# Kernel tuning notes

Hardware: AMD Instinct MI355X
Metric: run time of the kernel (lower is better)

## Reference

```python
import jax, jax.numpy as jnp
import numpy as np

N, E, F_IN, H, T, G, NCONV = 50000, 800000, 128, 64, 8, 64, 3
BN_EPS = 1e-5


def _bn_relu(h, gamma, beta):
    # BatchNorm1d in training mode: biased batch stats over the node dim
    m = h.mean(axis=0)
    v = h.var(axis=0)
    return jax.nn.relu(gamma * (h - m) * jax.lax.rsqrt(v + BN_EPS) + beta)


def _mlp(h, W1, b1, g1, be1, W2, b2, g2, be2):
    h = _bn_relu(h @ W1 + b1, g1, be1)
    return _bn_relu(h @ W2 + b2, g2, be2)


def setup_inputs() -> dict:
    key = jax.random.key(0)
    ks = jax.random.split(key, 12)
    x = jax.random.normal(ks[0], (N, F_IN), dtype=jnp.float32)
    edge_index = jax.random.randint(ks[1], (2, E), 0, N, dtype=jnp.int64)
    batch = jnp.sort(jax.random.randint(ks[2], (N,), 0, G, dtype=jnp.int64))
    s = 0.05
    inp = {
        "x": x, "edge_index": edge_index, "batch": batch,
        # first_h: Linear(F_IN,H)+BN+ReLU+Linear(H,H)+BN+ReLU
        "fh_W1": jax.random.normal(ks[3], (F_IN, H), jnp.float32) * s,
        "fh_b1": jnp.zeros((H,), jnp.float32),
        "fh_g1": jnp.ones((H,), jnp.float32),
        "fh_be1": jnp.zeros((H,), jnp.float32),
        "fh_W2": jax.random.normal(ks[4], (H, H), jnp.float32) * s,
        "fh_b2": jnp.zeros((H,), jnp.float32),
        "fh_g2": jnp.ones((H,), jnp.float32),
        "fh_be2": jnp.zeros((H,), jnp.float32),
        # stacked GINConv MLPs (all H->H)
        "cv_W1": jax.random.normal(ks[5], (NCONV, H, H), jnp.float32) * s,
        "cv_b1": jnp.zeros((NCONV, H), jnp.float32),
        "cv_g1": jnp.ones((NCONV, H), jnp.float32),
        "cv_be1": jnp.zeros((NCONV, H), jnp.float32),
        "cv_W2": jax.random.normal(ks[6], (NCONV, H, H), jnp.float32) * s,
        "cv_b2": jnp.zeros((NCONV, H), jnp.float32),
        "cv_g2": jnp.ones((NCONV, H), jnp.float32),
        "cv_be2": jnp.zeros((NCONV, H), jnp.float32),
        # per-layer readout linears (NCONV+1 of them)
        "lin_W": jax.random.normal(ks[7], (NCONV + 1, H, T), jnp.float32) * s,
        "lin_b": jnp.zeros((NCONV + 1, T), jnp.float32),
    }
    return inp


def reference(x, edge_index, batch, fh_W1, fh_b1, fh_g1, fh_be1, fh_W2, fh_b2,
              fh_g2, fh_be2, cv_W1, cv_b1, cv_g1, cv_be1, cv_W2, cv_b2, cv_g2,
              cv_be2, lin_W, lin_b):
    src, dst = edge_index[0], edge_index[1]
    eps = 0.0  # eps=0.0, train_eps=False
    # layer 0: first_h + pooled readout
    h = _mlp(x, fh_W1, fh_b1, fh_g1, fh_be1, fh_W2, fh_b2, fh_g2, fh_be2)
    out = jax.ops.segment_max(h @ lin_W[0] + lin_b[0], batch, num_segments=G)
    # GIN conv layers: neighbor sum-aggregation + MLP, with per-layer readout
    for l in range(NCONV):
        agg = jax.ops.segment_sum(h[src], dst, num_segments=N)  # [N,H]
        h = _mlp((1.0 + eps) * h + agg, cv_W1[l], cv_b1[l], cv_g1[l],
                 cv_be1[l], cv_W2[l], cv_b2[l], cv_g2[l], cv_be2[l])
        out = out + jax.ops.segment_max(h @ lin_W[l + 1] + lin_b[l + 1],
                                        batch, num_segments=G)
    return (out, h)
```

## Files before the change

### kernel.cpp

```cpp
#include <hip/hip_runtime.h>
#include <hip/hip_fp16.h>

#define NN 50000
#define EE 800000
#define FIN 128
#define HH 64
#define TT 8
#define GG 64
#define NCONVS 3
#define BN_EPS 1e-5f
#define RNODES 128
#define NBKT 196
#define SCAT_CHUNK 2048

__device__ __forceinline__ unsigned enc_f32(float x) {
  unsigned u = __float_as_uint(x);
  return (u & 0x80000000u) ? ~u : (u | 0x80000000u);
}
__device__ __forceinline__ float dec_f32(unsigned e) {
  unsigned u = (e & 0x80000000u) ? (e & 0x7fffffffu) : ~e;
  return __uint_as_float(u);
}

template <int K, int MODE>
__global__ __launch_bounds__(256) void mm_stats_kernel(
    const float* __restrict__ in, const __half* __restrict__ hin,
    const __half* __restrict__ agg, const float* __restrict__ stats_in,
    const float* __restrict__ gamma, const float* __restrict__ beta,
    const float* __restrict__ W, const float* __restrict__ bias,
    __half* __restrict__ y16, float* __restrict__ stats_out) {
  constexpr int NPH = K / 64;
  __shared__ float Wl[K * HH];
  __shared__ float AT[64 * 68];
  __shared__ float ssl[128];
  __shared__ float sred[4][128];
  const int t = threadIdx.x;
  if (MODE == 1) {
    if (t < 64) {
      const float inv = 1.f / (float)NN;
      const float mean = stats_in[t] * inv;
      const float var = stats_in[64 + t] * inv - mean * mean;
      const float sc = gamma[t] * rsqrtf(var + BN_EPS);
      ssl[t] = sc;
      ssl[64 + t] = fmaf(-mean, sc, beta[t]);
    }
    __syncthreads();
  }
  {
    const float4* W4 = (const float4*)W;
    float4* Wl4 = (float4*)Wl;
#pragma unroll
    for (int i = 0; i < (K * HH) / 1024; ++i) Wl4[t + i * 256] = W4[t + i * 256];
  }
  const int srow = t >> 2, scq = t & 3;
  const int grow_s = blockIdx.x * 64 + srow;
  const int g4 = (t & 15) * 4;
  const int r0 = (t >> 4) * 4;
  const int row0 = blockIdx.x * 64 + r0;
  const float4 bb = *(const float4*)&bias[g4];
  float4 acc0 = make_float4(0, 0, 0, 0), acc1 = make_float4(0, 0, 0, 0);
  float4 acc2 = make_float4(0, 0, 0, 0), acc3 = make_float4(0, 0, 0, 0);

#pragma unroll
  for (int p = 0; p < NPH; ++p) {
    if (p > 0) __syncthreads();
    if (MODE == 0) {
      if (grow_s < NN) {
#pragma unroll
        for (int i = 0; i < 4; ++i) {
          const int kl = scq * 16 + i * 4;
          const float4 v = *(const float4*)&in[(size_t)grow_s * K + p * 64 + kl];
          AT[(kl + 0) * 68 + srow] = v.x;
          AT[(kl + 1) * 68 + srow] = v.y;
          AT[(kl + 2) * 68 + srow] = v.z;
          AT[(kl + 3) * 68 + srow] = v.w;
        }
      } else {
#pragma unroll
        for (int i = 0; i < 16; ++i) AT[(scq * 16 + i) * 68 + srow] = 0.f;
      }
    } else {
      if (grow_s < NN) {
#pragma unroll
        for (int q = 0; q < 2; ++q) {
          const int kl = scq * 16 + q * 8;
          const int4 rv = *(const int4*)&hin[grow_s * HH + kl];
          const __half2* hp = (const __half2*)&rv;
          const float2 f0 = __half22float2(hp[0]);
          const float2 f1 = __half22float2(hp[1]);
          const float2 f2 = __half22float2(hp[2]);
          const float2 f3 = __half22float2(hp[3]);
          float f[8] = {f0.x, f0.y, f1.x, f1.y, f2.x, f2.y, f3.x, f3.y};
          if (MODE == 2) {
            const int4 av = *(const int4*)&agg[grow_s * HH + kl];
            const __half2* ap = (const __half2*)&av;
            const float2 a0 = __half22float2(ap[0]);
            const float2 a1 = __half22float2(ap[1]);
            const float2 a2 = __half22float2(ap[2]);
            const float2 a3 = __half22float2(ap[3]);
            f[0] += a0.x; f[1] += a0.y; f[2] += a1.x; f[3] += a1.y;
            f[4] += a2.x; f[5] += a2.y; f[6] += a3.x; f[7] += a3.y;
          } else {
#pragma unroll
            for (int j = 0; j < 8; ++j)
              f[j] = fmaxf(fmaf(f[j], ssl[kl + j], ssl[64 + kl + j]), 0.f);
          }
#pragma unroll
          for (int j = 0; j < 8; ++j) AT[(kl + j) * 68 + srow] = f[j];
        }
      } else {
#pragma unroll
        for (int i = 0; i < 16; ++i) AT[(scq * 16 + i) * 68 + srow] = 0.f;
      }
    }
    __syncthreads();
#pragma unroll 8
    for (int kl = 0; kl < 64; ++kl) {
      const float4 w = *(const float4*)&Wl[(p * 64 + kl) * HH + g4];
      const float4 a = *(const float4*)&AT[kl * 68 + r0];
      acc0.x = fmaf(a.x, w.x, acc0.x); acc0.y = fmaf(a.x, w.y, acc0.y);
      acc0.z = fmaf(a.x, w.z, acc0.z); acc0.w = fmaf(a.x, w.w, acc0.w);
      acc1.x = fmaf(a.y, w.x, acc1.x); acc1.y = fmaf(a.y, w.y, acc1.y);
      acc1.z = fmaf(a.y, w.z, acc1.z); acc1.w = fmaf(a.y, w.w, acc1.w);
      acc2.x = fmaf(a.z, w.x, acc2.x); acc2.y = fmaf(a.z, w.y, acc2.y);
      acc2.z = fmaf(a.z, w.z, acc2.z); acc2.w = fmaf(a.z, w.w, acc2.w);
      acc3.x = fmaf(a.w, w.x, acc3.x); acc3.y = fmaf(a.w, w.y, acc3.y);
      acc3.z = fmaf(a.w, w.z, acc3.z); acc3.w = fmaf(a.w, w.w, acc3.w);
    }
  }
  float st_s[4] = {0.f, 0.f, 0.f, 0.f}, st_q[4] = {0.f, 0.f, 0.f, 0.f};
#pragma unroll
  for (int ri = 0; ri < 4; ++ri) {
    const int grow = row0 + ri;
    if (grow < NN) {
      const float4 ac = (ri == 0) ? acc0 : (ri == 1) ? acc1 : (ri == 2) ? acc2 : acc3;
      float4 o;
      o.x = ac.x + bb.x; o.y = ac.y + bb.y; o.z = ac.z + bb.z; o.w = ac.w + bb.w;
      const __half2 p0 = __floats2half2_rn(o.x, o.y);
      const __half2 p1 = __floats2half2_rn(o.z, o.w);
      int2 pk;
      pk.x = *(const int*)&p0; pk.y = *(const int*)&p1;
      *(int2*)&y16[grow * HH + g4] = pk;
      st_s[0] += o.x; st_s[1] += o.y; st_s[2] += o.z; st_s[3] += o.w;
      st_q[0] = fmaf(o.x, o.x, st_q[0]); st_q[1] = fmaf(o.y, o.y, st_q[1]);
      st_q[2] = fmaf(o.z, o.z, st_q[2]); st_q[3] = fmaf(o.w, o.w, st_q[3]);
    }
  }
#pragma unroll
  for (int off = 16; off <= 32; off <<= 1) {
#pragma unroll
    for (int i = 0; i < 4; ++i) {
      st_s[i] += __shfl_xor(st_s[i], off);
      st_q[i] += __shfl_xor(st_q[i], off);
    }
  }
  const int wave = t >> 6, lane = t & 63;
  if (lane < 16) {
#pragma unroll
    for (int i = 0; i < 4; ++i) {
      sred[wave][lane * 4 + i] = st_s[i];
      sred[wave][64 + lane * 4 + i] = st_q[i];
    }
  }
  __syncthreads();
  if (t < 128)
    atomicAdd(&stats_out[t],
              sred[0][t] + sred[1][t] + sred[2][t] + sred[3][t]);
}

__global__ __launch_bounds__(256) void bcount_kernel(const int* __restrict__ ei,
                                                     int* __restrict__ bcnt) {
  __shared__ int l[256];
  const int t = threadIdx.x;
  l[t] = 0;
  __syncthreads();
  for (int e = blockIdx.x * 256 + t; e < EE; e += gridDim.x * 256)
    atomicAdd(&l[ei[EE + e] >> 8], 1);
  __syncthreads();
  if (t < NBKT && l[t]) atomicAdd(&bcnt[t], l[t]);
}

__global__ void bscan_kernel(const int* __restrict__ bcnt,
                             int* __restrict__ bbase, int* __restrict__ bcur) {
  __shared__ int s[256];
  const int t = threadIdx.x;
  const int v = (t < NBKT) ? bcnt[t] : 0;
  s[t] = v;
  __syncthreads();
  for (int off = 1; off < 256; off <<= 1) {
    const int u = (t >= off) ? s[t - off] : 0;
    __syncthreads();
    s[t] += u;
    __syncthreads();
  }
  const int excl = s[t] - v;
  if (t < NBKT) {
    bbase[t] = excl;
    bcur[t] = excl;
  }
  if (t == 255) bbase[NBKT] = s[255];
}

__global__ __launch_bounds__(256) void bscatter_kernel(
    const int* __restrict__ ei, int* __restrict__ bcur,
    unsigned long long* __restrict__ ebuf) {
  __shared__ int lcnt[256];
  __shared__ int lbase[256];
  const int t = threadIdx.x;
  lcnt[t] = 0;
  __syncthreads();
  const int e0 = blockIdx.x * SCAT_CHUNK;
  int mysrc[8], mydl[8], mybkt[8], myloc[8];
#pragma unroll
  for (int i = 0; i < 8; ++i) {
    const int e = e0 + i * 256 + t;
    if (e < EE) {
      const int dst = ei[EE + e];
      mybkt[i] = dst >> 8;
      mydl[i] = dst & 255;
      mysrc[i] = ei[e];
      myloc[i] = atomicAdd(&lcnt[mybkt[i]], 1);
    } else {
      mybkt[i] = -1;
    }
  }
  __syncthreads();
  if (t < NBKT && lcnt[t]) lbase[t] = atomicAdd(&bcur[t], lcnt[t]);
  __syncthreads();
#pragma unroll
  for (int i = 0; i < 8; ++i) {
    if (mybkt[i] >= 0) {
      const int pos = lbase[mybkt[i]] + myloc[i];
      ebuf[pos] = ((unsigned long long)(unsigned)mydl[i] << 32) |
                  (unsigned)mysrc[i];
    }
  }
}

__global__ __launch_bounds__(256) void bcsr_kernel(
    const int* __restrict__ bbase, const unsigned long long* __restrict__ ebuf,
    int* __restrict__ offs, int* __restrict__ srcs) {
  __shared__ int ldeg[256];
  __shared__ int sscan[256];
  __shared__ int lcur[256];
  const int t = threadIdx.x;
  const int b = blockIdx.x;
  const int e0 = bbase[b], e1 = bbase[b + 1];
  ldeg[t] = 0;
  __syncthreads();
  for (int e = e0 + t; e < e1; e += 256)
    atomicAdd(&ldeg[(int)(ebuf[e] >> 32)], 1);
  __syncthreads();
  const int v = ldeg[t];
  sscan[t] = v;
  __syncthreads();
  for (int off = 1; off < 256; off <<= 1) {
    const int u = (t >= off) ? sscan[t - off] : 0;
    __syncthreads();
    sscan[t] += u;
    __syncthreads();
  }
  const int excl = sscan[t] - v;
  const int node = b * 256 + t;
  if (node < NN) offs[node] = e0 + excl;
  if (b == NBKT - 1 && t == 0) offs[NN] = EE;
  lcur[t] = e0 + excl;
  __syncthreads();
  for (int e = e0 + t; e < e1; e += 256) {
    const unsigned long long u = ebuf[e];
    const int dl = (int)(u >> 32);
    const int pos = atomicAdd(&lcur[dl], 1);
    srcs[pos] = (int)(u & 0xffffffffu);
  }
}

__device__ __forceinline__ void acc_half8(const int4 r, float4& lo, float4& hi) {
  const __half2* p = (const __half2*)&r;
  const float2 f0 = __half22float2(p[0]);
  const float2 f1 = __half22float2(p[1]);
  const float2 f2 = __half22float2(p[2]);
  const float2 f3 = __half22float2(p[3]);
  lo.x += f0.x; lo.y += f0.y; lo.z += f1.x; lo.w += f1.y;
  hi.x += f2.x; hi.y += f2.y; hi.z += f3.x; hi.w += f3.y;
}

__global__ __launch_bounds__(256) void gather16_kernel(
    const int* __restrict__ offs, const int* __restrict__ srcs,
    const __half* __restrict__ h16, __half* __restrict__ agg) {
  const int gid = blockIdx.x * 256 + threadIdx.x;
  const int n = gid >> 3, lane = gid & 7;
  if (n >= NN) return;
  const int c0 = lane * 8;
  const int s0 = offs[n], s1 = offs[n + 1];
  float4 aA0 = make_float4(0, 0, 0, 0), aA1 = make_float4(0, 0, 0, 0);
  float4 aB0 = make_float4(0, 0, 0, 0), aB1 = make_float4(0, 0, 0, 0);
  int j = s0;
  for (; j + 1 < s1; j += 2) {
    const int sA = srcs[j], sB = srcs[j + 1];
    const int4 rA = *(const int4*)&h16[sA * HH + c0];
    const int4 rB = *(const int4*)&h16[sB * HH + c0];
    acc_half8(rA, aA0, aA1);
    acc_half8(rB, aB0, aB1);
  }
  if (j < s1) {
    const int4 rA = *(const int4*)&h16[srcs[j] * HH + c0];
    acc_half8(rA, aA0, aA1);
  }
  aA0.x += aB0.x; aA0.y += aB0.y; aA0.z += aB0.z; aA0.w += aB0.w;
  aA1.x += aB1.x; aA1.y += aB1.y; aA1.z += aB1.z; aA1.w += aB1.w;
  const __half2 p0 = __floats2half2_rn(aA0.x, aA0.y);
  const __half2 p1 = __floats2half2_rn(aA0.z, aA0.w);
  const __half2 p2 = __floats2half2_rn(aA1.x, aA1.y);
  const __half2 p3 = __floats2half2_rn(aA1.z, aA1.w);
  int4 pk;
  pk.x = *(const int*)&p0; pk.y = *(const int*)&p1;
  pk.z = *(const int*)&p2; pk.w = *(const int*)&p3;
  *(int4*)&agg[n * HH + c0] = pk;
}

template <int WMODE>
__global__ __launch_bounds__(256) void bnrelu_readout_kernel(
    const __half* __restrict__ y2, const float* __restrict__ stats_in,
    const float* __restrict__ gamma, const float* __restrict__ beta,
    float* __restrict__ hout, __half* __restrict__ h16out,
    const float* __restrict__ linW, const float* __restrict__ linb,
    const int* __restrict__ batch, unsigned* __restrict__ outmax) {
  __shared__ float Wl[HH * 9];
  __shared__ float lb[8];
  __shared__ float ssl[128];
  __shared__ unsigned smax[8][8];
  const int t = threadIdx.x;
  if (t < 64) {
#pragma unroll
    for (int j = 0; j < 8; ++j) Wl[t * 9 + j] = linW[t * 8 + j];
    const float inv = 1.f / (float)NN;
    const float mean = stats_in[t] * inv;
    const float var = stats_in[64 + t] * inv - mean * mean;
    const float sc = gamma[t] * rsqrtf(var + BN_EPS);
    ssl[t] = sc;
    ssl[64 + t] = fmaf(-mean, sc, beta[t]);
  }
  if (t < 8) lb[t] = linb[t];
  if (t >= 64 && t < 128) smax[(t - 64) >> 3][(t - 64) & 7] = 0u;
  const int gfirst = batch[blockIdx.x * RNODES < NN ? blockIdx.x * RNODES : NN - 1];
  __syncthreads();
  const int nl = t >> 3;
  const int c0 = (t & 7) * 8;
  const int b0 = t & 1, b1 = (t >> 1) & 1, b2 = (t >> 2) & 1;
#pragma unroll
  for (int chunk = 0; chunk < RNODES / 32; ++chunk) {
    const int n = blockIdx.x * RNODES + chunk * 32 + nl;
    if (n < NN) {
      float hv[8];
      {
        const int4 rv = *(const int4*)&y2[n * HH + c0];
        const __half2* hp = (const __half2*)&rv;
        const float2 f0 = __half22float2(hp[0]);
        const float2 f1 = __half22float2(hp[1]);
        const float2 f2 = __half22float2(hp[2]);
        const float2 f3 = __half22float2(hp[3]);
        hv[0] = fmaxf(fmaf(f0.x, ssl[c0 + 0], ssl[64 + c0 + 0]), 0.f);
        hv[1] = fmaxf(fmaf(f0.y, ssl[c0 + 1], ssl[64 + c0 + 1]), 0.f);
        hv[2] = fmaxf(fmaf(f1.x, ssl[c0 + 2], ssl[64 + c0 + 2]), 0.f);
        hv[3] = fmaxf(fmaf(f1.y, ssl[c0 + 3], ssl[64 + c0 + 3]), 0.f);
        hv[4] = fmaxf(fmaf(f2.x, ssl[c0 + 4], ssl[64 + c0 + 4]), 0.f);
        hv[5] = fmaxf(fmaf(f2.y, ssl[c0 + 5], ssl[64 + c0 + 5]), 0.f);
        hv[6] = fmaxf(fmaf(f3.x, ssl[c0 + 6], ssl[64 + c0 + 6]), 0.f);
        hv[7] = fmaxf(fmaf(f3.y, ssl[c0 + 7], ssl[64 + c0 + 7]), 0.f);
      }
      if (WMODE == 1) {
        *(float4*)&hout[n * HH + c0] = make_float4(hv[0], hv[1], hv[2], hv[3]);
        *(float4*)&hout[n * HH + c0 + 4] = make_float4(hv[4], hv[5], hv[6], hv[7]);
      } else {
        const __half2 p0 = __floats2half2_rn(hv[0], hv[1]);
        const __half2 p1 = __floats2half2_rn(hv[2], hv[3]);
        const __half2 p2 = __floats2half2_rn(hv[4], hv[5]);
        const __half2 p3 = __floats2half2_rn(hv[6], hv[7]);
        int4 pk;
        pk.x = *(const int*)&p0; pk.y = *(const int*)&p1;
        pk.z = *(const int*)&p2; pk.w = *(const int*)&p3;
        *(int4*)&h16out[n * HH + c0] = pk;
      }
      float rr[8] = {0, 0, 0, 0, 0, 0, 0, 0};
#pragma unroll
      for (int j = 0; j < 8; ++j) {
        const float a = hv[j];
        const int k = c0 + j;
#pragma unroll
        for (int u = 0; u < 8; ++u) rr[u] = fmaf(a, Wl[k * 9 + u], rr[u]);
      }
      float s4[4];
#pragma unroll
      for (int i = 0; i < 4; ++i) {
        const float keepv = b0 ? rr[2 * i + 1] : rr[2 * i];
        const float send = b0 ? rr[2 * i] : rr[2 * i + 1];
        s4[i] = keepv + __shfl_xor(send, 1);
      }
      float s2[2];
#pragma unroll
      for (int i = 0; i < 2; ++i) {
        const float keepv = b1 ? s4[2 * i + 1] : s4[2 * i];
        const float send = b1 ? s4[2 * i] : s4[2 * i + 1];
        s2[i] = keepv + __shfl_xor(send, 2);
      }
      const float keepv = b2 ? s2[1] : s2[0];
      const float send = b2 ? s2[0] : s2[1];
      const float v = keepv + __shfl_xor(send, 4) + lb[t & 7];
      const int g = batch[n];
      const int gidx = g - gfirst;
      const unsigned ev = enc_f32(v);
      if (gidx < 8)
        atomicMax(&smax[gidx][t & 7], ev);
      else
        atomicMax(&outmax[g * 8 + (t & 7)], ev);
    }
  }
  __syncthreads();
  if (t < 64) {
    const unsigned vv = smax[t >> 3][t & 7];
    if (vv) atomicMax(&outmax[(gfirst + (t >> 3)) * 8 + (t & 7)], vv);
  }
}

__global__ void combine_kernel(const unsigned* __restrict__ outmax,
                               float* __restrict__ out) {
  const int i = blockIdx.x * 64 + threadIdx.x;
  float s = 0.f;
#pragma unroll
  for (int l = 0; l < 4; ++l) s += dec_f32(outmax[l * GG * TT + i]);
  out[i] = s;
}

extern "C" void kernel_launch(void* const* d_in, const int* in_sizes, int n_in,
                              void* d_out, int out_size, void* d_ws,
                              size_t ws_size, hipStream_t stream) {
  const float* x      = (const float*)d_in[0];
  const int*   ei     = (const int*)d_in[1];
  const int*   batch  = (const int*)d_in[2];
  const float* fh_W1  = (const float*)d_in[3];
  const float* fh_b1  = (const float*)d_in[4];
  const float* fh_g1  = (const float*)d_in[5];
  const float* fh_be1 = (const float*)d_in[6];
  const float* fh_W2  = (const float*)d_in[7];
  const float* fh_b2  = (const float*)d_in[8];
  const float* fh_g2  = (const float*)d_in[9];
  const float* fh_be2 = (const float*)d_in[10];
  const float* cv_W1  = (const float*)d_in[11];
  const float* cv_b1  = (const float*)d_in[12];
  const float* cv_g1  = (const float*)d_in[13];
  const float* cv_be1 = (const float*)d_in[14];
  const float* cv_W2  = (const float*)d_in[15];
  const float* cv_b2  = (const float*)d_in[16];
  const float* cv_g2  = (const float*)d_in[17];
  const float* cv_be2 = (const float*)d_in[18];
  const float* lin_W  = (const float*)d_in[19];
  const float* lin_b  = (const float*)d_in[20];

  float* out = (float*)d_out;
  float* h = out + GG * TT;

  char* w = (char*)d_ws;
  float* stats = (float*)w;                       w += 8 * 128 * 4;
  unsigned* outmax = (unsigned*)w;                w += 4 * GG * TT * 4;
  int* bcnt = (int*)w;                            w += 256 * 4;
  int* bbase = (int*)w;                           w += 256 * 4;
  int* bcur = (int*)w;                            w += 256 * 4;
  int* offs = (int*)w;                            w += (NN + 1) * 4;
  int* srcs = (int*)w;                            w += (size_t)EE * 4;
  w = (char*)(((size_t)w + 15) & ~(size_t)15);
  __half* h16 = (__half*)w;                       w += (size_t)NN * HH * 2;
  __half* y1 = (__half*)w;                        w += (size_t)NN * HH * 2;
  __half* y2 = (__half*)w;                        w += (size_t)NN * HH * 2;
  w = (char*)(((size_t)w + 15) & ~(size_t)15);
  __half* agg = (__half*)w;                       w += (size_t)NN * HH * 2;
  unsigned long long* ebuf = (unsigned long long*)agg;

  const int NBLK = (NN + 63) / 64;
  const int NRD = (NN + RNODES - 1) / RNODES;
  const int NGA = (NN * 8 + 255) / 256;
  const int NSC = (EE + SCAT_CHUNK - 1) / SCAT_CHUNK;

  hipMemsetAsync(stats, 0, (8 * 128 + 4 * GG * TT) * sizeof(float), stream);
  hipMemsetAsync(bcnt, 0, 256 * sizeof(int), stream);

  bcount_kernel<<<512, 256, 0, stream>>>(ei, bcnt);
  bscan_kernel<<<1, 256, 0, stream>>>(bcnt, bbase, bcur);
  bscatter_kernel<<<NSC, 256, 0, stream>>>(ei, bcur, ebuf);
  bcsr_kernel<<<NBKT, 256, 0, stream>>>(bbase, ebuf, offs, srcs);

  mm_stats_kernel<FIN, 0><<<NBLK, 256, 0, stream>>>(
      x, nullptr, nullptr, nullptr, nullptr, nullptr, fh_W1, fh_b1, y1, stats);
  mm_stats_kernel<HH, 1><<<NBLK, 256, 0, stream>>>(
      nullptr, y1, nullptr, stats, fh_g1, fh_be1, fh_W2, fh_b2, y2, stats + 128);
  bnrelu_readout_kernel<0><<<NRD, 256, 0, stream>>>(
      y2, stats + 128, fh_g2, fh_be2, h, h16, lin_W, lin_b, batch, outmax);

  for (int l = 0; l < NCONVS; ++l) {
    float* s1 = stats + (2 + 2 * l) * 128;
    float* s2 = stats + (3 + 2 * l) * 128;
    gather16_kernel<<<NGA, 256, 0, stream>>>(offs, srcs, h16, agg);
    mm_stats_kernel<HH, 2><<<NBLK, 256, 0, stream>>>(
        nullptr, h16, agg, nullptr, nullptr, nullptr,
        cv_W1 + l * HH * HH, cv_b1 + l * HH, y1, s1);
    mm_stats_kernel<HH, 1><<<NBLK, 256, 0, stream>>>(
        nullptr, y1, nullptr, s1, cv_g1 + l * HH, cv_be1 + l * HH,
        cv_W2 + l * HH * HH, cv_b2 + l * HH, y2, s2);
    if (l == NCONVS - 1) {
      bnrelu_readout_kernel<1><<<NRD, 256, 0, stream>>>(
          y2, s2, cv_g2 + l * HH, cv_be2 + l * HH, h, h16,
          lin_W + (l + 1) * HH * TT, lin_b + (l + 1) * TT, batch,
          outmax + (l + 1) * GG * TT);
    } else {
      bnrelu_readout_kernel<0><<<NRD, 256, 0, stream>>>(
          y2, s2, cv_g2 + l * HH, cv_be2 + l * HH, h, h16,
          lin_W + (l + 1) * HH * TT, lin_b + (l + 1) * TT, batch,
          outmax + (l + 1) * GG * TT);
    }
  }
  combine_kernel<<<8, 64, 0, stream>>>(outmax, out);
}
```

Before: 362.3 us.

## Fuse BN+ReLU into gather and GEMM loads, use fp16 dot2 GEMM

Removes the h16 intermediate: the readout kernel no longer writes a half-precision copy of h. Instead the gather kernel and the first conv GEMM apply the previous layer's BN+ReLU on the fly from y2 and its stats. The GEMM kernel moves to 128-thread blocks, stores W and activations as packed half2 in LDS, and accumulates with v_dot2 fp16 instructions over a 4x8 register tile. This cuts a full N×H write and read per layer and halves LDS traffic. In exchange, BN is recomputed per gathered edge, fp16 rounding is added to the first-layer input x and the weights, and RNODES and the memsets are also adjusted.

After: 363.9 us. No clear change (+0.4%).

```diff
diff --git a/kernel.cpp b/kernel.cpp
--- a/kernel.cpp
+++ b/kernel.cpp
@@ -9,9 +9,11 @@
 #define GG 64
 #define NCONVS 3
 #define BN_EPS 1e-5f
-#define RNODES 128
+#define RNODES 64
 #define NBKT 196
 #define SCAT_CHUNK 2048
+
+typedef _Float16 h2f __attribute__((ext_vector_type(2)));
 
 __device__ __forceinline__ unsigned enc_f32(float x) {
   unsigned u = __float_as_uint(x);
@@ -22,20 +24,32 @@
   return __uint_as_float(u);
 }
 
+__device__ __forceinline__ float fdot2f(int a, int b, float c) {
+#if __has_builtin(__builtin_amdgcn_fdot2)
+  return __builtin_amdgcn_fdot2(__builtin_bit_cast(h2f, a),
+                                __builtin_bit_cast(h2f, b), c, false);
+#else
+  const __half2 ha = __builtin_bit_cast(__half2, a);
+  const __half2 hb = __builtin_bit_cast(__half2, b);
+  const float2 fa = __half22float2(ha), fb = __half22float2(hb);
+  return fmaf(fa.y, fb.y, fmaf(fa.x, fb.x, c));
+#endif
+}
+
 template <int K, int MODE>
-__global__ __launch_bounds__(256) void mm_stats_kernel(
+__global__ __launch_bounds__(128) void mm_stats_kernel(
     const float* __restrict__ in, const __half* __restrict__ hin,
     const __half* __restrict__ agg, const float* __restrict__ stats_in,
     const float* __restrict__ gamma, const float* __restrict__ beta,
     const float* __restrict__ W, const float* __restrict__ bias,
     __half* __restrict__ y16, float* __restrict__ stats_out) {
   constexpr int NPH = K / 64;
-  __shared__ float Wl[K * HH];
-  __shared__ float AT[64 * 68];
+  __shared__ __half2 Wl2[(K / 2) * HH];
+  __shared__ __half2 AT2[32 * 68];
   __shared__ float ssl[128];
-  __shared__ float sred[4][128];
-  const int t = threadIdx.x;
-  if (MODE == 1) {
+  __shared__ float sred[2][128];
+  const int t = threadIdx.x;
+  if (MODE != 0) {
     if (t < 64) {
       const float inv = 1.f / (float)NN;
       const float mean = stats_in[t] * inv;
@@ -46,53 +60,54 @@
     }
     __syncthreads();
   }
-  {
-    const float4* W4 = (const float4*)W;
-    float4* Wl4 = (float4*)Wl;
-#pragma unroll
-    for (int i = 0; i < (K * HH) / 1024; ++i) Wl4[t + i * 256] = W4[t + i * 256];
-  }
-  const int srow = t >> 2, scq = t & 3;
+#pragma unroll
+  for (int i = 0; i < K / 4; ++i) {
+    const int idx = t + i * 128;
+    const int kk = idx >> 6, c = idx & 63;
+    Wl2[idx] = __floats2half2_rn(W[(2 * kk) * HH + c], W[(2 * kk + 1) * HH + c]);
+  }
+  const int srow = t >> 1, shalf = t & 1;
   const int grow_s = blockIdx.x * 64 + srow;
-  const int g4 = (t & 15) * 4;
-  const int r0 = (t >> 4) * 4;
-  const int row0 = blockIdx.x * 64 + r0;
-  const float4 bb = *(const float4*)&bias[g4];
-  float4 acc0 = make_float4(0, 0, 0, 0), acc1 = make_float4(0, 0, 0, 0);
-  float4 acc2 = make_float4(0, 0, 0, 0), acc3 = make_float4(0, 0, 0, 0);
+  const int cg = t & 7, rg = t >> 3;
+  const int c0 = cg * 8, r0 = rg * 4;
+  float acc[4][8] = {};
 
 #pragma unroll
   for (int p = 0; p < NPH; ++p) {
     if (p > 0) __syncthreads();
-    if (MODE == 0) {
-      if (grow_s < NN) {
-#pragma unroll
-        for (int i = 0; i < 4; ++i) {
-          const int kl = scq * 16 + i * 4;
-          const float4 v = *(const float4*)&in[(size_t)grow_s * K + p * 64 + kl];
-          AT[(kl + 0) * 68 + srow] = v.x;
-          AT[(kl + 1) * 68 + srow] = v.y;
-          AT[(kl + 2) * 68 + srow] = v.z;
-          AT[(kl + 3) * 68 + srow] = v.w;
+    if (grow_s < NN) {
+      if (MODE == 0) {
+#pragma unroll
+        for (int q = 0; q < 4; ++q) {
+          const int cc = p * 64 + shalf * 32 + q * 8;
+          const float4 v0 = *(const float4*)&in[(size_t)grow_s * K + cc];
+          const float4 v1 = *(const float4*)&in[(size_t)grow_s * K + cc + 4];
+          const int kk = shalf * 16 + q * 4;
+          AT2[(kk + 0) * 68 + srow] = __floats2half2_rn(v0.x, v0.y);
+          AT2[(kk + 1) * 68 + srow] = __floats2half2_rn(v0.z, v0.w);
+          AT2[(kk + 2) * 68 + srow] = __floats2half2_rn(v1.x, v1.y);
+          AT2[(kk + 3) * 68 + srow] = __floats2half2_rn(v1.z, v1.w);
         }
       } else {
 #pragma unroll
-        for (int i = 0; i < 16; ++i) AT[(scq * 16 + i) * 68 + srow] = 0.f;
-      }
-    } else {
-      if (grow_s < NN) {
-#pragma unroll
-        for (int q = 0; q < 2; ++q) {
-          const int kl = scq * 16 + q * 8;
-          const int4 rv = *(const int4*)&hin[grow_s * HH + kl];
+        for (int q = 0; q < 4; ++q) {
+          const int cc = shalf * 32 + q * 8;
+          const int4 rv = *(const int4*)&hin[grow_s * HH + cc];
           const __half2* hp = (const __half2*)&rv;
-          const float2 f0 = __half22float2(hp[0]);
-          const float2 f1 = __half22float2(hp[1]);
-          const float2 f2 = __half22float2(hp[2]);
-          const float2 f3 = __half22float2(hp[3]);
-          float f[8] = {f0.x, f0.y, f1.x, f1.y, f2.x, f2.y, f3.x, f3.y};
+          float f[8];
+          {
+            const float2 f0 = __half22float2(hp[0]);
+            const float2 f1 = __half22float2(hp[1]);
+            const float2 f2 = __half22float2(hp[2]);
+            const float2 f3 = __half22float2(hp[3]);
+            f[0] = f0.x; f[1] = f0.y; f[2] = f1.x; f[3] = f1.y;
+            f[4] = f2.x; f[5] = f2.y; f[6] = f3.x; f[7] = f3.y;
+          }
+#pragma unroll
+          for (int j = 0; j < 8; ++j)
+            f[j] = fmaxf(fmaf(f[j], ssl[cc + j], ssl[64 + cc + j]), 0.f);
           if (MODE == 2) {
-            const int4 av = *(const int4*)&agg[grow_s * HH + kl];
+            const int4 av = *(const int4*)&agg[grow_s * HH + cc];
             const __half2* ap = (const __half2*)&av;
             const float2 a0 = __half22float2(ap[0]);
             const float2 a1 = __half22float2(ap[1]);
@@ -100,72 +115,78 @@
             const float2 a3 = __half22float2(ap[3]);
             f[0] += a0.x; f[1] += a0.y; f[2] += a1.x; f[3] += a1.y;
             f[4] += a2.x; f[5] += a2.y; f[6] += a3.x; f[7] += a3.y;
-          } else {
-#pragma unroll
-            for (int j = 0; j < 8; ++j)
-              f[j] = fmaxf(fmaf(f[j], ssl[kl + j], ssl[64 + kl + j]), 0.f);
           }
-#pragma unroll
-          for (int j = 0; j < 8; ++j) AT[(kl + j) * 68 + srow] = f[j];
+          const int kk = shalf * 16 + q * 4;
+          AT2[(kk + 0) * 68 + srow] = __floats2half2_rn(f[0], f[1]);
+          AT2[(kk + 1) * 68 + srow] = __floats2half2_rn(f[2], f[3]);
+          AT2[(kk + 2) * 68 + srow] = __floats2half2_rn(f[4], f[5]);
+          AT2[(kk + 3) * 68 + srow] = __floats2half2_rn(f[6], f[7]);
         }
-      } else {
-#pragma unroll
-        for (int i = 0; i < 16; ++i) AT[(scq * 16 + i) * 68 + srow] = 0.f;
-      }
+      }
+    } else {
+      const __half2 z = __floats2half2_rn(0.f, 0.f);
+#pragma unroll
+      for (int i2 = 0; i2 < 16; ++i2) AT2[(shalf * 16 + i2) * 68 + srow] = z;
     }
     __syncthreads();
 #pragma unroll 8
-    for (int kl = 0; kl < 64; ++kl) {
-      const float4 w = *(const float4*)&Wl[(p * 64 + kl) * HH + g4];
-      const float4 a = *(const float4*)&AT[kl * 68 + r0];
-      acc0.x = fmaf(a.x, w.x, acc0.x); acc0.y = fmaf(a.x, w.y, acc0.y);
-      acc0.z = fmaf(a.x, w.z, acc0.z); acc0.w = fmaf(a.x, w.w, acc0.w);
-      acc1.x = fmaf(a.y, w.x, acc1.x); acc1.y = fmaf(a.y, w.y, acc1.y);
-      acc1.z = fmaf(a.y, w.z, acc1.z); acc1.w = fmaf(a.y, w.w, acc1.w);
-      acc2.x = fmaf(a.z, w.x, acc2.x); acc2.y = fmaf(a.z, w.y, acc2.y);
-      acc2.z = fmaf(a.z, w.z, acc2.z); acc2.w = fmaf(a.z, w.w, acc2.w);
-      acc3.x = fmaf(a.w, w.x, acc3.x); acc3.y = fmaf(a.w, w.y, acc3.y);
-      acc3.z = fmaf(a.w, w.z, acc3.z); acc3.w = fmaf(a.w, w.w, acc3.w);
-    }
-  }
-  float st_s[4] = {0.f, 0.f, 0.f, 0.f}, st_q[4] = {0.f, 0.f, 0.f, 0.f};
+    for (int kk = 0; kk < 32; ++kk) {
+      const int4 w0 = *(const int4*)&Wl2[(p * 32 + kk) * HH + c0];
+      const int4 w1 = *(const int4*)&Wl2[(p * 32 + kk) * HH + c0 + 4];
+      const int4 av = *(const int4*)&AT2[kk * 68 + r0];
+      const int wu[8] = {w0.x, w0.y, w0.z, w0.w, w1.x, w1.y, w1.z, w1.w};
+      const int au[4] = {av.x, av.y, av.z, av.w};
+#pragma unroll
+      for (int r = 0; r < 4; ++r)
+#pragma unroll
+        for (int c = 0; c < 8; ++c)
+          acc[r][c] = fdot2f(au[r], wu[c], acc[r][c]);
+    }
+  }
+  const float4 bb0 = *(const float4*)&bias[c0];
+  const float4 bb1 = *(const float4*)&bias[c0 + 4];
+  const float bbv[8] = {bb0.x, bb0.y, bb0.z, bb0.w, bb1.x, bb1.y, bb1.z, bb1.w};
+  float st_s[8] = {}, st_q[8] = {};
+  const int row0 = blockIdx.x * 64 + r0;
 #pragma unroll
   for (int ri = 0; ri < 4; ++ri) {
     const int grow = row0 + ri;
     if (grow < NN) {
-      const float4 ac = (ri == 0) ? acc0 : (ri == 1) ? acc1 : (ri == 2) ? acc2 : acc3;
-      float4 o;
-      o.x = ac.x + bb.x; o.y = ac.y + bb.y; o.z = ac.z + bb.z; o.w = ac.w + bb.w;
-      const __half2 p0 = __floats2half2_rn(o.x, o.y);
-      const __half2 p1 = __floats2half2_rn(o.z, o.w);
-      int2 pk;
+      float o[8];
+#pragma unroll
+      for (int c = 0; c < 8; ++c) {
+        o[c] = acc[ri][c] + bbv[c];
+        st_s[c] += o[c];
+        st_q[c] = fmaf(o[c], o[c], st_q[c]);
+      }
+      const __half2 p0 = __floats2half2_rn(o[0], o[1]);
+      const __half2 p1 = __floats2half2_rn(o[2], o[3]);
+      const __half2 p2 = __floats2half2_rn(o[4], o[5]);
+      const __half2 p3 = __floats2half2_rn(o[6], o[7]);
+      int4 pk;
       pk.x = *(const int*)&p0; pk.y = *(const int*)&p1;
-      *(int2*)&y16[grow * HH + g4] = pk;
-      st_s[0] += o.x; st_s[1] += o.y; st_s[2] += o.z; st_s[3] += o.w;
-      st_q[0] = fmaf(o.x, o.x, st_q[0]); st_q[1] = fmaf(o.y, o.y, st_q[1]);
-      st_q[2] = fmaf(o.z, o.z, st_q[2]); st_q[3] = fmaf(o.w, o.w, st_q[3]);
-    }
-  }
-#pragma unroll
-  for (int off = 16; off <= 32; off <<= 1) {
-#pragma unroll
-    for (int i = 0; i < 4; ++i) {
-      st_s[i] += __shfl_xor(st_s[i], off);
-      st_q[i] += __shfl_xor(st_q[i], off);
+      pk.z = *(const int*)&p2; pk.w = *(const int*)&p3;
+      *(int4*)&y16[grow * HH + c0] = pk;
+    }
+  }
+#pragma unroll
+  for (int off = 8; off <= 32; off <<= 1) {
+#pragma unroll
+    for (int c = 0; c < 8; ++c) {
+      st_s[c] += __shfl_xor(st_s[c], off);
+      st_q[c] += __shfl_xor(st_q[c], off);
     }
   }
   const int wave = t >> 6, lane = t & 63;
-  if (lane < 16) {
-#pragma unroll
-    for (int i = 0; i < 4; ++i) {
-      sred[wave][lane * 4 + i] = st_s[i];
-      sred[wave][64 + lane * 4 + i] = st_q[i];
-    }
-  }
-  __syncthreads();
-  if (t < 128)
-    atomicAdd(&stats_out[t],
-              sred[0][t] + sred[1][t] + sred[2][t] + sred[3][t]);
+  if (lane < 8) {
+#pragma unroll
+    for (int c = 0; c < 8; ++c) {
+      sred[wave][lane * 8 + c] = st_s[c];
+      sred[wave][64 + lane * 8 + c] = st_q[c];
+    }
+  }
+  __syncthreads();
+  if (t < 128) atomicAdd(&stats_out[t], sred[0][t] + sred[1][t]);
 }
 
 __global__ __launch_bounds__(256) void bcount_kernel(const int* __restrict__ ei,
@@ -274,44 +295,55 @@
   }
 }
 
-__device__ __forceinline__ void acc_half8(const int4 r, float4& lo, float4& hi) {
-  const __half2* p = (const __half2*)&r;
-  const float2 f0 = __half22float2(p[0]);
-  const float2 f1 = __half22float2(p[1]);
-  const float2 f2 = __half22float2(p[2]);
-  const float2 f3 = __half22float2(p[3]);
-  lo.x += f0.x; lo.y += f0.y; lo.z += f1.x; lo.w += f1.y;
-  hi.x += f2.x; hi.y += f2.y; hi.z += f3.x; hi.w += f3.y;
-}
-
 __global__ __launch_bounds__(256) void gather16_kernel(
     const int* __restrict__ offs, const int* __restrict__ srcs,
-    const __half* __restrict__ h16, __half* __restrict__ agg) {
-  const int gid = blockIdx.x * 256 + threadIdx.x;
+    const __half* __restrict__ y, const float* __restrict__ stats_in,
+    const float* __restrict__ gamma, const float* __restrict__ beta,
+    __half* __restrict__ agg) {
+  __shared__ float ssl[128];
+  const int t = threadIdx.x;
+  if (t < 64) {
+    const float inv = 1.f / (float)NN;
+    const float mean = stats_in[t] * inv;
+    const float var = stats_in[64 + t] * inv - mean * mean;
+    const float sc = gamma[t] * rsqrtf(var + BN_EPS);
+    ssl[t] = sc;
+    ssl[64 + t] = fmaf(-mean, sc, beta[t]);
+  }
+  __syncthreads();
+  const int gid = blockIdx.x * 256 + t;
   const int n = gid >> 3, lane = gid & 7;
   if (n >= NN) return;
   const int c0 = lane * 8;
+  float sc[8], sh[8];
+#pragma unroll
+  for (int j = 0; j < 8; ++j) {
+    sc[j] = ssl[c0 + j];
+    sh[j] = ssl[64 + c0 + j];
+  }
   const int s0 = offs[n], s1 = offs[n + 1];
-  float4 aA0 = make_float4(0, 0, 0, 0), aA1 = make_float4(0, 0, 0, 0);
-  float4 aB0 = make_float4(0, 0, 0, 0), aB1 = make_float4(0, 0, 0, 0);
-  int j = s0;
-  for (; j + 1 < s1; j += 2) {
-    const int sA = srcs[j], sB = srcs[j + 1];
-    const int4 rA = *(const int4*)&h16[sA * HH + c0];
-    const int4 rB = *(const int4*)&h16[sB * HH + c0];
-    acc_half8(rA, aA0, aA1);
-    acc_half8(rB, aB0, aB1);
-  }
-  if (j < s1) {
-    const int4 rA = *(const int4*)&h16[srcs[j] * HH + c0];
-    acc_half8(rA, aA0, aA1);
-  }
-  aA0.x += aB0.x; aA0.y += aB0.y; aA0.z += aB0.z; aA0.w += aB0.w;
-  aA1.x += aB1.x; aA1.y += aB1.y; aA1.z += aB1.z; aA1.w += aB1.w;
-  const __half2 p0 = __floats2half2_rn(aA0.x, aA0.y);
-  const __half2 p1 = __floats2half2_rn(aA0.z, aA0.w);
-  const __half2 p2 = __floats2half2_rn(aA1.x, aA1.y);
-  const __half2 p3 = __floats2half2_rn(aA1.z, aA1.w);
+  float a[8] = {};
+#pragma unroll 2
+  for (int j = s0; j < s1; ++j) {
+    const int4 rv = *(const int4*)&y[srcs[j] * HH + c0];
+    const __half2* hp = (const __half2*)&rv;
+    const float2 f0 = __half22float2(hp[0]);
+    const float2 f1 = __half22float2(hp[1]);
+    const float2 f2 = __half22float2(hp[2]);
+    const float2 f3 = __half22float2(hp[3]);
+    a[0] += fmaxf(fmaf(f0.x, sc[0], sh[0]), 0.f);
+    a[1] += fmaxf(fmaf(f0.y, sc[1], sh[1]), 0.f);
+    a[2] += fmaxf(fmaf(f1.x, sc[2], sh[2]), 0.f);
+    a[3] += fmaxf(fmaf(f1.y, sc[3], sh[3]), 0.f);
+    a[4] += fmaxf(fmaf(f2.x, sc[4], sh[4]), 0.f);
+    a[5] += fmaxf(fmaf(f2.y, sc[5], sh[5]), 0.f);
+    a[6] += fmaxf(fmaf(f3.x, sc[6], sh[6]), 0.f);
+    a[7] += fmaxf(fmaf(f3.y, sc[7], sh[7]), 0.f);
+  }
+  const __half2 p0 = __floats2half2_rn(a[0], a[1]);
+  const __half2 p1 = __floats2half2_rn(a[2], a[3]);
+  const __half2 p2 = __floats2half2_rn(a[4], a[5]);
+  const __half2 p3 = __floats2half2_rn(a[6], a[7]);
   int4 pk;
   pk.x = *(const int*)&p0; pk.y = *(const int*)&p1;
   pk.z = *(const int*)&p2; pk.w = *(const int*)&p3;
@@ -322,9 +354,9 @@
 __global__ __launch_bounds__(256) void bnrelu_readout_kernel(
     const __half* __restrict__ y2, const float* __restrict__ stats_in,
     const float* __restrict__ gamma, const float* __restrict__ beta,
-    float* __restrict__ hout, __half* __restrict__ h16out,
-    const float* __restrict__ linW, const float* __restrict__ linb,
-    const int* __restrict__ batch, unsigned* __restrict__ outmax) {
+    float* __restrict__ hout, const float* __restrict__ linW,
+    const float* __restrict__ linb, const int* __restrict__ batch,
+    unsigned* __restrict__ outmax) {
   __shared__ float Wl[HH * 9];
   __shared__ float lb[8];
   __shared__ float ssl[128];
@@ -371,15 +403,6 @@
       if (WMODE == 1) {
         *(float4*)&hout[n * HH + c0] = make_float4(hv[0], hv[1], hv[2], hv[3]);
         *(float4*)&hout[n * HH + c0 + 4] = make_float4(hv[4], hv[5], hv[6], hv[7]);
-      } else {
-        const __half2 p0 = __floats2half2_rn(hv[0], hv[1]);
-        const __half2 p1 = __floats2half2_rn(hv[2], hv[3]);
-        const __half2 p2 = __floats2half2_rn(hv[4], hv[5]);
-        const __half2 p3 = __floats2half2_rn(hv[6], hv[7]);
-        int4 pk;
-        pk.x = *(const int*)&p0; pk.y = *(const int*)&p1;
-        pk.z = *(const int*)&p2; pk.w = *(const int*)&p3;
-        *(int4*)&h16out[n * HH + c0] = pk;
       }
       float rr[8] = {0, 0, 0, 0, 0, 0, 0, 0};
 #pragma unroll
@@ -468,7 +491,6 @@
   int* offs = (int*)w;                            w += (NN + 1) * 4;
   int* srcs = (int*)w;                            w += (size_t)EE * 4;
   w = (char*)(((size_t)w + 15) & ~(size_t)15);
-  __half* h16 = (__half*)w;                       w += (size_t)NN * HH * 2;
   __half* y1 = (__half*)w;                        w += (size_t)NN * HH * 2;
   __half* y2 = (__half*)w;                        w += (size_t)NN * HH * 2;
   w = (char*)(((size_t)w + 15) & ~(size_t)15);
@@ -480,39 +502,44 @@
   const int NGA = (NN * 8 + 255) / 256;
   const int NSC = (EE + SCAT_CHUNK - 1) / SCAT_CHUNK;
 
-  hipMemsetAsync(stats, 0, (8 * 128 + 4 * GG * TT) * sizeof(float), stream);
-  hipMemsetAsync(bcnt, 0, 256 * sizeof(int), stream);
+  hipMemsetAsync(stats, 0, (8 * 128 + 4 * GG * TT + 256) * sizeof(float),
+                 stream);
 
   bcount_kernel<<<512, 256, 0, stream>>>(ei, bcnt);
   bscan_kernel<<<1, 256, 0, stream>>>(bcnt, bbase, bcur);
   bscatter_kernel<<<NSC, 256, 0, stream>>>(ei, bcur, ebuf);
   bcsr_kernel<<<NBKT, 256, 0, stream>>>(bbase, ebuf, offs, srcs);
 
-  mm_stats_kernel<FIN, 0><<<NBLK, 256, 0, stream>>>(
+  mm_stats_kernel<FIN, 0><<<NBLK, 128, 0, stream>>>(
       x, nullptr, nullptr, nullptr, nullptr, nullptr, fh_W1, fh_b1, y1, stats);
-  mm_stats_kernel<HH, 1><<<NBLK, 256, 0, stream>>>(
-      nullptr, y1, nullptr, stats, fh_g1, fh_be1, fh_W2, fh_b2, y2, stats + 128);
+  mm_stats_kernel<HH, 1><<<NBLK, 128, 0, stream>>>(
+      nullptr, y1, nullptr, stats, fh_g1, fh_be1, fh_W2, fh_b2, y2,
+      stats + 128);
   bnrelu_readout_kernel<0><<<NRD, 256, 0, stream>>>(
-      y2, stats + 128, fh_g2, fh_be2, h, h16, lin_W, lin_b, batch, outmax);
+      y2, stats + 128, fh_g2, fh_be2, h, lin_W, lin_b, batch, outmax);
 
   for (int l = 0; l < NCONVS; ++l) {
-    float* s1 = stats + (2 + 2 * l) * 128;
-    float* s2 = stats + (3 + 2 * l) * 128;
-    gather16_kernel<<<NGA, 256, 0, stream>>>(offs, srcs, h16, agg);
-    mm_stats_kernel<HH, 2><<<NBLK, 256, 0, stream>>>(
-        nullptr, h16, agg, nullptr, nullptr, nullptr,
-        cv_W1 + l * HH * HH, cv_b1 + l * HH, y1, s1);
-    mm_stats_kernel<HH, 1><<<NBLK, 256, 0, stream>>>(
-        nullptr, y1, nullptr, s1, cv_g1 + l * HH, cv_be1 + l * HH,
-        cv_W2 + l * HH * HH, cv_b2 + l * HH, y2, s2);
+    float* sprev = stats + (1 + 2 * l) * 128;
+    float* sA = stats + (2 + 2 * l) * 128;
+    float* sB = stats + (3 + 2 * l) * 128;
+    const float* pg = (l == 0) ? fh_g2 : cv_g2 + (l - 1) * HH;
+    const float* pb = (l == 0) ? fh_be2 : cv_be2 + (l - 1) * HH;
+    gather16_kernel<<<NGA, 256, 0, stream>>>(offs, srcs, y2, sprev, pg, pb,
+                                             agg);
+    mm_stats_kernel<HH, 2><<<NBLK, 128, 0, stream>>>(
+        nullptr, y2, agg, sprev, pg, pb, cv_W1 + l * HH * HH, cv_b1 + l * HH,
+        y1, sA);
+    mm_stats_kernel<HH, 1><<<NBLK, 128, 0, stream>>>(
+        nullptr, y1, nullptr, sA, cv_g1 + l * HH, cv_be1 + l * HH,
+        cv_W2 + l * HH * HH, cv_b2 + l * HH, y2, sB);
     if (l == NCONVS - 1) {
       bnrelu_readout_kernel<1><<<NRD, 256, 0, stream>>>(
-          y2, s2, cv_g2 + l * HH, cv_be2 + l * HH, h, h16,
+          y2, sB, cv_g2 + l * HH, cv_be2 + l * HH, h,
           lin_W + (l + 1) * HH * TT, lin_b + (l + 1) * TT, batch,
           outmax + (l + 1) * GG * TT);
     } else {
       bnrelu_readout_kernel<0><<<NRD, 256, 0, stream>>>(
-          y2, s2, cv_g2 + l * HH, cv_be2 + l * HH, h, h16,
+          y2, sB, cv_g2 + l * HH, cv_be2 + l * HH, h,
           lin_W + (l + 1) * HH * TT, lin_b + (l + 1) * TT, batch,
           outmax + (l + 1) * GG * TT);
     }
```
